# Performance work log

Measured on AMD Instinct MI355X. Metric: run time of the kernel, lower is better.

The kernel has to match this reference:

```python
import jax, jax.numpy as jnp
import numpy as np
from jax.scipy.special import logsumexp

TAU = 1.0
N_ITERS = 20
D = 1024
B = 65536


def setup_inputs() -> dict:
    key = jax.random.key(0)
    k1, k2 = jax.random.split(key)
    embeddings = jax.random.normal(k1, (B, D), dtype=jnp.float32)
    log_scores = jax.random.normal(k2, (D, D), dtype=jnp.float32) * 0.01
    return {"embeddings": embeddings, "log_scores": log_scores}


def _sinkhorn(log_alpha):
    # 20 alternating row/column logsumexp normalizations on a (d, d) matrix
    def body(_, la):
        la = la - logsumexp(la, axis=-1, keepdims=True)  # row normalize
        la = la - logsumexp(la, axis=-2, keepdims=True)  # col normalize
        return la
    log_alpha = jax.lax.fori_loop(0, N_ITERS, body, log_alpha)
    return jnp.exp(log_alpha)


def reference(embeddings, log_scores):
    P = _sinkhorn(log_scores / TAU)           # (d, d) approx doubly stochastic
    # (P @ embeddings.T).T == embeddings @ P.T
    return embeddings @ P.T                   # (B, d)
```

## Files before the change

kernel.cpp:

```cpp
#include <hip/hip_runtime.h>
#include <hip/hip_bf16.h>

#define D_DIM 1024
#define NITER 20

typedef float f32x4 __attribute__((ext_vector_type(4)));
typedef __bf16 bf16x4 __attribute__((ext_vector_type(4)));
typedef __bf16 bf16x8 __attribute__((ext_vector_type(8)));

__global__ __launch_bounds__(1024)
void prep_exp_transpose(const float* __restrict__ ls, float* __restrict__ Mm,
                        float* __restrict__ Mt) {
    __shared__ float tile[64][65];
    const int tx = threadIdx.x, ty = threadIdx.y;
    const int bx = blockIdx.x * 64, by = blockIdx.y * 64;
#pragma unroll
    for (int k = 0; k < 64; k += 16) {
        int r = by + ty + k, c = bx + tx;
        float v = expf(ls[r * D_DIM + c]);
        Mm[r * D_DIM + c] = v;
        tile[ty + k][tx] = v;
    }
    __syncthreads();
#pragma unroll
    for (int k = 0; k < 64; k += 16) {
        int r = bx + ty + k, c = by + tx;
        Mt[r * D_DIM + c] = tile[tx][ty + k];
    }
}

__global__ void init_u(float* u) { u[threadIdx.x] = 1.0f; }

__global__ __launch_bounds__(256)
void matvec_recip(const float* __restrict__ A, const float* __restrict__ x,
                  float* __restrict__ y) {
    const int wave = threadIdx.x >> 6, lane = threadIdx.x & 63;
    const int row = blockIdx.x * 4 + wave;
    const f32x4* Ar = (const f32x4*)(A + row * D_DIM);
    const f32x4* xr = (const f32x4*)x;
    float s = 0.f;
#pragma unroll
    for (int it = 0; it < 4; ++it) {
        f32x4 a = Ar[lane + it * 64];
        f32x4 b = xr[lane + it * 64];
        s += a.x * b.x + a.y * b.y + a.z * b.z + a.w * b.w;
    }
#pragma unroll
    for (int off = 32; off > 0; off >>= 1) s += __shfl_down(s, off, 64);
    if (lane == 0) y[row] = 1.0f / s;
}

__global__ __launch_bounds__(256)
void finalize_P(const float* __restrict__ Mm, const float* __restrict__ r,
                const float* __restrict__ u, __bf16* __restrict__ P) {
    const int i = blockIdx.x;
    const int t = threadIdx.x;
    const float ri = r[i];
    f32x4 m = ((const f32x4*)(Mm + i * D_DIM))[t];
    f32x4 uu = ((const f32x4*)u)[t];
    bf16x4 o;
    o[0] = (__bf16)(m.x * ri * uu.x);
    o[1] = (__bf16)(m.y * ri * uu.y);
    o[2] = (__bf16)(m.z * ri * uu.z);
    o[3] = (__bf16)(m.w * ri * uu.w);
    ((bf16x4*)(P + i * D_DIM))[t] = o;
}

#define BM 128
#define BN 128
#define BK 32

__global__ __launch_bounds__(256)
void gemm_a32_bt16(const float* __restrict__ A, const __bf16* __restrict__ Bt,
                   float* __restrict__ C, int Msz, int Nsz, int Ksz) {
    __shared__ __bf16 As[BM * BK];
    __shared__ __bf16 Bs[BN * BK];
    const int tid = threadIdx.x;
    const int wave = tid >> 6, lane = tid & 63;
    const int wm = wave >> 1, wn = wave & 1;
    const int quad = lane >> 4, l16 = lane & 15;
    const int m0 = blockIdx.y * BM, n0 = blockIdx.x * BN;

    f32x4 acc[4][4] = {};

    for (int k0 = 0; k0 < Ksz; k0 += BK) {
        __syncthreads();
#pragma unroll
        for (int it = 0; it < 4; ++it) {
            int idx = tid + it * 256;
            int row = idx >> 3, kq = idx & 7;
            f32x4 v = *(const f32x4*)(A + (size_t)(m0 + row) * Ksz + k0 + kq * 4);
            bf16x4 b;
            b[0] = (__bf16)v.x; b[1] = (__bf16)v.y;
            b[2] = (__bf16)v.z; b[3] = (__bf16)v.w;
            *(bf16x4*)(&As[row * BK + kq * 4]) = b;
        }
#pragma unroll
        for (int q = 0; q < 2; ++q) {
            int t8 = wave * 2 + q;
            int nrow = t8 * 16 + (lane >> 2);
            const __bf16* g = Bt + (size_t)(n0 + nrow) * Ksz + k0 + (lane & 3) * 8;
            __bf16* l = Bs + t8 * 512;
            __builtin_amdgcn_global_load_lds(
                (const __attribute__((address_space(1))) void*)g,
                (__attribute__((address_space(3))) void*)l, 16, 0, 0);
        }
        __syncthreads();

        bf16x8 af[4], bfr[4];
#pragma unroll
        for (int a = 0; a < 4; ++a)
            af[a] = *(const bf16x8*)(&As[(wm * 64 + a * 16 + l16) * BK + quad * 8]);
#pragma unroll
        for (int b = 0; b < 4; ++b)
            bfr[b] = *(const bf16x8*)(&Bs[(wn * 64 + b * 16 + l16) * BK + quad * 8]);
#pragma unroll
        for (int a = 0; a < 4; ++a)
#pragma unroll
            for (int b = 0; b < 4; ++b)
                acc[a][b] = __builtin_amdgcn_mfma_f32_16x16x32_bf16(
                    af[a], bfr[b], acc[a][b], 0, 0, 0);
    }

#pragma unroll
    for (int a = 0; a < 4; ++a) {
        int mg = m0 + wm * 64 + a * 16 + quad * 4;
#pragma unroll
        for (int b = 0; b < 4; ++b) {
            int ng = n0 + wn * 64 + b * 16 + l16;
#pragma unroll
            for (int v = 0; v < 4; ++v)
                C[(size_t)(mg + v) * Nsz + ng] = acc[a][b][v];
        }
    }
}

extern "C" void kernel_launch(void* const* d_in, const int* in_sizes, int n_in,
                              void* d_out, int out_size, void* d_ws, size_t ws_size,
                              hipStream_t stream) {
    const float* emb = (const float*)d_in[0];
    const float* ls  = (const float*)d_in[1];
    float* out = (float*)d_out;
    char* ws = (char*)d_ws;

    float* Mm  = (float*)ws;
    float* Mt  = (float*)(ws + (4u << 20));
    float* r   = (float*)(ws + (8u << 20));
    float* u   = (float*)(ws + (8u << 20) + 4096);
    __bf16* P  = (__bf16*)(ws + (8u << 20) + 8192);

    const int B = in_sizes[0] / D_DIM;

    prep_exp_transpose<<<dim3(16, 16), dim3(64, 16), 0, stream>>>(ls, Mm, Mt);
    init_u<<<1, D_DIM, 0, stream>>>(u);
    for (int it = 0; it < NITER; ++it) {
        matvec_recip<<<D_DIM / 4, 256, 0, stream>>>(Mm, u, r);
        matvec_recip<<<D_DIM / 4, 256, 0, stream>>>(Mt, r, u);
    }
    finalize_P<<<D_DIM, 256, 0, stream>>>(Mm, r, u, P);
    gemm_a32_bt16<<<dim3(D_DIM / BN, B / BM), 256, 0, stream>>>(
        emb, P, out, B, D_DIM, D_DIM);
}
```

Measured before the change: 742.2 us.

## Fuse Sinkhorn into one cooperative kernel and restructure GEMM with wider N tiles

The prep, 40 matvec and finalize launches are replaced by a single cooperative kernel that keeps each wave's rows of M and M^T in registers and separates the row and column steps with grid.sync(). The GEMM now gives each block a 128-row strip of embeddings and loops over all N in 256-wide tiles, with XOR-swizzled LDS layouts for the A and B fragments. The fusion removes launch overhead and repeated reads of M from global memory. Cost and risk: grid-wide syncs, fewer blocks in the GEMM grid, and each block re-reading and re-converting its fp32 A strip once per N tile.

```diff
diff --git a/kernel.cpp b/kernel.cpp
--- a/kernel.cpp
+++ b/kernel.cpp
@@ -1,5 +1,8 @@
 #include <hip/hip_runtime.h>
 #include <hip/hip_bf16.h>
+#include <hip/hip_cooperative_groups.h>
+
+namespace cg = cooperative_groups;
 
 #define D_DIM 1024
 #define NITER 20
@@ -8,66 +11,93 @@
 typedef __bf16 bf16x4 __attribute__((ext_vector_type(4)));
 typedef __bf16 bf16x8 __attribute__((ext_vector_type(8)));
 
-__global__ __launch_bounds__(1024)
-void prep_exp_transpose(const float* __restrict__ ls, float* __restrict__ Mm,
-                        float* __restrict__ Mt) {
-    __shared__ float tile[64][65];
-    const int tx = threadIdx.x, ty = threadIdx.y;
-    const int bx = blockIdx.x * 64, by = blockIdx.y * 64;
-#pragma unroll
-    for (int k = 0; k < 64; k += 16) {
-        int r = by + ty + k, c = bx + tx;
-        float v = expf(ls[r * D_DIM + c]);
-        Mm[r * D_DIM + c] = v;
-        tile[ty + k][tx] = v;
-    }
-    __syncthreads();
-#pragma unroll
-    for (int k = 0; k < 64; k += 16) {
-        int r = bx + ty + k, c = by + tx;
-        Mt[r * D_DIM + c] = tile[tx][ty + k];
+__global__ __launch_bounds__(256)
+void sinkhorn_fused(const float* __restrict__ ls, float* __restrict__ Mm,
+                    float* __restrict__ Mt, float* __restrict__ r,
+                    float* __restrict__ u, __bf16* __restrict__ P) {
+    cg::grid_group grid = cg::this_grid();
+    const int tid = threadIdx.x, bid = blockIdx.x;
+    const int wave = tid >> 6, lane = tid & 63;
+
+    {
+        __shared__ float tile[64][65];
+        const int bx = (bid & 15) * 64, by = (bid >> 4) * 64;
+        const int tx = tid & 63, ty = tid >> 6;
+#pragma unroll
+        for (int k = 0; k < 64; k += 4) {
+            int row = by + ty + k;
+            float v = expf(ls[row * D_DIM + bx + tx]);
+            Mm[row * D_DIM + bx + tx] = v;
+            tile[ty + k][tx] = v;
+        }
+        if (bid == 0) {
+            f32x4 one = {1.f, 1.f, 1.f, 1.f};
+            ((f32x4*)u)[tid] = one;
+        }
+        __syncthreads();
+#pragma unroll
+        for (int k = 0; k < 64; k += 4) {
+            int row = bx + ty + k;
+            Mt[row * D_DIM + by + tx] = tile[tx][ty + k];
+        }
+    }
+    grid.sync();
+
+    const int row = bid * 4 + wave;
+    const f32x4* Ar  = (const f32x4*)(Mm + (size_t)row * D_DIM);
+    const f32x4* Atr = (const f32x4*)(Mt + (size_t)row * D_DIM);
+    f32x4 am[4], at[4];
+#pragma unroll
+    for (int q = 0; q < 4; ++q) {
+        am[q] = Ar[lane + q * 64];
+        at[q] = Atr[lane + q * 64];
+    }
+    for (int it = 0; it < NITER; ++it) {
+        {
+            const f32x4* xr = (const f32x4*)u;
+            float s = 0.f;
+#pragma unroll
+            for (int q = 0; q < 4; ++q) {
+                f32x4 b = xr[lane + q * 64];
+                s += am[q].x * b.x + am[q].y * b.y + am[q].z * b.z + am[q].w * b.w;
+            }
+#pragma unroll
+            for (int off = 32; off; off >>= 1) s += __shfl_down(s, off, 64);
+            if (lane == 0) r[row] = 1.0f / s;
+        }
+        grid.sync();
+        {
+            const f32x4* xr = (const f32x4*)r;
+            float s = 0.f;
+#pragma unroll
+            for (int q = 0; q < 4; ++q) {
+                f32x4 b = xr[lane + q * 64];
+                s += at[q].x * b.x + at[q].y * b.y + at[q].z * b.z + at[q].w * b.w;
+            }
+#pragma unroll
+            for (int off = 32; off; off >>= 1) s += __shfl_down(s, off, 64);
+            if (lane == 0) u[row] = 1.0f / s;
+        }
+        grid.sync();
+    }
+
+#pragma unroll
+    for (int rr = 0; rr < 4; ++rr) {
+        int i = bid * 4 + rr;
+        float ri = r[i];
+        f32x4 m = ((const f32x4*)(Mm + (size_t)i * D_DIM))[tid];
+        f32x4 uu = ((const f32x4*)u)[tid];
+        bf16x4 o;
+        o[0] = (__bf16)(m.x * ri * uu.x);
+        o[1] = (__bf16)(m.y * ri * uu.y);
+        o[2] = (__bf16)(m.z * ri * uu.z);
+        o[3] = (__bf16)(m.w * ri * uu.w);
+        ((bf16x4*)(P + (size_t)i * D_DIM))[tid] = o;
     }
 }
 
-__global__ void init_u(float* u) { u[threadIdx.x] = 1.0f; }
-
-__global__ __launch_bounds__(256)
-void matvec_recip(const float* __restrict__ A, const float* __restrict__ x,
-                  float* __restrict__ y) {
-    const int wave = threadIdx.x >> 6, lane = threadIdx.x & 63;
-    const int row = blockIdx.x * 4 + wave;
-    const f32x4* Ar = (const f32x4*)(A + row * D_DIM);
-    const f32x4* xr = (const f32x4*)x;
-    float s = 0.f;
-#pragma unroll
-    for (int it = 0; it < 4; ++it) {
-        f32x4 a = Ar[lane + it * 64];
-        f32x4 b = xr[lane + it * 64];
-        s += a.x * b.x + a.y * b.y + a.z * b.z + a.w * b.w;
-    }
-#pragma unroll
-    for (int off = 32; off > 0; off >>= 1) s += __shfl_down(s, off, 64);
-    if (lane == 0) y[row] = 1.0f / s;
-}
-
-__global__ __launch_bounds__(256)
-void finalize_P(const float* __restrict__ Mm, const float* __restrict__ r,
-                const float* __restrict__ u, __bf16* __restrict__ P) {
-    const int i = blockIdx.x;
-    const int t = threadIdx.x;
-    const float ri = r[i];
-    f32x4 m = ((const f32x4*)(Mm + i * D_DIM))[t];
-    f32x4 uu = ((const f32x4*)u)[t];
-    bf16x4 o;
-    o[0] = (__bf16)(m.x * ri * uu.x);
-    o[1] = (__bf16)(m.y * ri * uu.y);
-    o[2] = (__bf16)(m.z * ri * uu.z);
-    o[3] = (__bf16)(m.w * ri * uu.w);
-    ((bf16x4*)(P + i * D_DIM))[t] = o;
-}
-
 #define BM 128
-#define BN 128
+#define BN 256
 #define BK 32
 
 __global__ __launch_bounds__(256)
@@ -79,58 +109,66 @@
     const int wave = tid >> 6, lane = tid & 63;
     const int wm = wave >> 1, wn = wave & 1;
     const int quad = lane >> 4, l16 = lane & 15;
-    const int m0 = blockIdx.y * BM, n0 = blockIdx.x * BN;
-
-    f32x4 acc[4][4] = {};
-
-    for (int k0 = 0; k0 < Ksz; k0 += BK) {
-        __syncthreads();
-#pragma unroll
-        for (int it = 0; it < 4; ++it) {
-            int idx = tid + it * 256;
-            int row = idx >> 3, kq = idx & 7;
-            f32x4 v = *(const f32x4*)(A + (size_t)(m0 + row) * Ksz + k0 + kq * 4);
-            bf16x4 b;
-            b[0] = (__bf16)v.x; b[1] = (__bf16)v.y;
-            b[2] = (__bf16)v.z; b[3] = (__bf16)v.w;
-            *(bf16x4*)(&As[row * BK + kq * 4]) = b;
-        }
-#pragma unroll
-        for (int q = 0; q < 2; ++q) {
-            int t8 = wave * 2 + q;
-            int nrow = t8 * 16 + (lane >> 2);
-            const __bf16* g = Bt + (size_t)(n0 + nrow) * Ksz + k0 + (lane & 3) * 8;
-            __bf16* l = Bs + t8 * 512;
-            __builtin_amdgcn_global_load_lds(
-                (const __attribute__((address_space(1))) void*)g,
-                (__attribute__((address_space(3))) void*)l, 16, 0, 0);
-        }
-        __syncthreads();
-
-        bf16x8 af[4], bfr[4];
-#pragma unroll
-        for (int a = 0; a < 4; ++a)
-            af[a] = *(const bf16x8*)(&As[(wm * 64 + a * 16 + l16) * BK + quad * 8]);
-#pragma unroll
-        for (int b = 0; b < 4; ++b)
-            bfr[b] = *(const bf16x8*)(&Bs[(wn * 64 + b * 16 + l16) * BK + quad * 8]);
-#pragma unroll
-        for (int a = 0; a < 4; ++a)
-#pragma unroll
-            for (int b = 0; b < 4; ++b)
-                acc[a][b] = __builtin_amdgcn_mfma_f32_16x16x32_bf16(
-                    af[a], bfr[b], acc[a][b], 0, 0, 0);
-    }
-
-#pragma unroll
-    for (int a = 0; a < 4; ++a) {
-        int mg = m0 + wm * 64 + a * 16 + quad * 4;
-#pragma unroll
-        for (int b = 0; b < 4; ++b) {
-            int ng = n0 + wn * 64 + b * 16 + l16;
-#pragma unroll
-            for (int v = 0; v < 4; ++v)
-                C[(size_t)(mg + v) * Nsz + ng] = acc[a][b][v];
+    const int m0 = blockIdx.x * BM;
+    const int sR = (l16 >> 1) & 3;
+
+    for (int bx = 0; bx < Nsz / BN; ++bx) {
+        const int n0 = bx * BN;
+        f32x4 acc[4][8] = {};
+        for (int k0 = 0; k0 < Ksz; k0 += BK) {
+            __syncthreads();
+#pragma unroll
+            for (int itc = 0; itc < 4; ++itc) {
+                int idx = tid + itc * 256;
+                int arow = idx >> 3, kq = idx & 7;
+                f32x4 v = *(const f32x4*)(A + (size_t)(m0 + arow) * Ksz + k0 + kq * 4);
+                bf16x4 b;
+                b[0] = (__bf16)v.x; b[1] = (__bf16)v.y;
+                b[2] = (__bf16)v.z; b[3] = (__bf16)v.w;
+                int slot = (kq >> 1) ^ ((arow >> 1) & 3);
+                *(bf16x4*)(&As[arow * BK + slot * 8 + (kq & 1) * 4]) = b;
+            }
+#pragma unroll
+            for (int q = 0; q < 4; ++q) {
+                int t = wave * 4 + q;
+                int nrow = t * 16 + (lane >> 2);
+                int kb = (lane & 3) ^ ((lane >> 3) & 3);
+                const __bf16* g = Bt + (size_t)(n0 + nrow) * Ksz + k0 + kb * 8;
+                __bf16* l = Bs + t * 512;
+                __builtin_amdgcn_global_load_lds(
+                    (const __attribute__((address_space(1))) void*)g,
+                    (__attribute__((address_space(3))) void*)l, 16, 0, 0);
+            }
+            __syncthreads();
+
+            bf16x8 af[4], bfr[8];
+#pragma unroll
+            for (int a = 0; a < 4; ++a) {
+                int arow = wm * 64 + a * 16 + l16;
+                af[a] = *(const bf16x8*)(&As[arow * BK + (quad ^ sR) * 8]);
+            }
+#pragma unroll
+            for (int b = 0; b < 8; ++b) {
+                int brow = wn * 128 + b * 16 + l16;
+                bfr[b] = *(const bf16x8*)(&Bs[brow * BK + (quad ^ sR) * 8]);
+            }
+#pragma unroll
+            for (int a = 0; a < 4; ++a)
+#pragma unroll
+                for (int b = 0; b < 8; ++b)
+                    acc[a][b] = __builtin_amdgcn_mfma_f32_16x16x32_bf16(
+                        af[a], bfr[b], acc[a][b], 0, 0, 0);
+        }
+#pragma unroll
+        for (int a = 0; a < 4; ++a) {
+            int mg = m0 + wm * 64 + a * 16 + quad * 4;
+#pragma unroll
+            for (int b = 0; b < 8; ++b) {
+                int ng = n0 + wn * 128 + b * 16 + l16;
+#pragma unroll
+                for (int v = 0; v < 4; ++v)
+                    C[(size_t)(mg + v) * Nsz + ng] = acc[a][b][v];
+            }
         }
     }
 }
@@ -151,13 +189,15 @@
 
     const int B = in_sizes[0] / D_DIM;
 
-    prep_exp_transpose<<<dim3(16, 16), dim3(64, 16), 0, stream>>>(ls, Mm, Mt);
-    init_u<<<1, D_DIM, 0, stream>>>(u);
-    for (int it = 0; it < NITER; ++it) {
-        matvec_recip<<<D_DIM / 4, 256, 0, stream>>>(Mm, u, r);
-        matvec_recip<<<D_DIM / 4, 256, 0, stream>>>(Mt, r, u);
-    }
-    finalize_P<<<D_DIM, 256, 0, stream>>>(Mm, r, u, P);
-    gemm_a32_bt16<<<dim3(D_DIM / BN, B / BM), 256, 0, stream>>>(
-        emb, P, out, B, D_DIM, D_DIM);
+    void* cargs[6];
+    cargs[0] = (void*)&ls;
+    cargs[1] = (void*)&Mm;
+    cargs[2] = (void*)&Mt;
+    cargs[3] = (void*)&r;
+    cargs[4] = (void*)&u;
+    cargs[5] = (void*)&P;
+    hipLaunchCooperativeKernel(sinkhorn_fused, dim3(256), dim3(256), cargs, 0,
+                               stream);
+
+    gemm_a32_bt16<<<dim3(B / BM), 256, 0, stream>>>(emb, P, out, B, D_DIM, D_DIM);
 }
```

Measured after the change: 1.851 ms. +149.4%, slower.
